# Kernel optimization log

Measured on AMD Instinct MI355X. Metric: run time of the kernel, lower is better.

The kernel has to match this reference:

```python
import math
import jax, jax.numpy as jnp
import numpy as np

B, Q, HID = 4, 4, 4096
NH, NKV, HD = 32, 8, 128
GROUPS = NH // NKV
CACHE_LEN = 4096
CACHE_MAX = CACHE_LEN + 512  # prefill_len + max_len(512)
ROPE_THETA = 500000.0
SCALE = 1.0 / math.sqrt(128.0)  # hardcoded softmax_scale in module


def rotate_half(x):
    x1, x2 = jnp.split(x, 2, axis=-1)
    return jnp.concatenate([-x2, x1], axis=-1)


def setup_inputs() -> dict:
    key = jax.random.key(0)
    ks = jax.random.split(key, 8)
    std = 0.02
    # RoPE angles for positions [CACHE_LEN, CACHE_LEN+Q)
    pos = (CACHE_LEN + jnp.arange(Q)).astype(jnp.float32)
    inv_freq = 1.0 / (ROPE_THETA ** (jnp.arange(0, HD, 2, dtype=jnp.float32) / HD))
    freqs = pos[:, None] * inv_freq[None, :]            # [Q, HD/2]
    emb = jnp.concatenate([freqs, freqs], axis=-1)      # [Q, HD]
    cos = jnp.broadcast_to(jnp.cos(emb)[None], (B, Q, HD)).astype(jnp.float32)
    sin = jnp.broadcast_to(jnp.sin(emb)[None], (B, Q, HD)).astype(jnp.float32)
    return {
        "hidden_states": jax.random.normal(ks[0], (B, Q, HID), jnp.float32),
        "cos": cos,
        "sin": sin,
        "K_Cache": jax.random.normal(ks[1], (B, NKV, CACHE_MAX, HD), jnp.float32) * 0.5,
        "V_Cache": jax.random.normal(ks[2], (B, NKV, CACHE_MAX, HD), jnp.float32) * 0.5,
        "Wq": jax.random.normal(ks[3], (NH * HD, HID), jnp.float32) * std,
        "Wk": jax.random.normal(ks[4], (NKV * HD, HID), jnp.float32) * std,
        "Wv": jax.random.normal(ks[5], (NKV * HD, HID), jnp.float32) * std,
        "Wo": jax.random.normal(ks[6], (HID, NH * HD), jnp.float32) * std,
        "cache_lens": int(CACHE_LEN),
    }


def reference(hidden_states, cos, sin, K_Cache, V_Cache, Wq, Wk, Wv, Wo, cache_lens):
    b, q, _ = hidden_states.shape
    # projections (torch Linear: x @ W.T), reshape to [b, h, q, d]
    qs = jnp.einsum('bsh,oh->bso', hidden_states, Wq).reshape(b, q, NH, HD).transpose(0, 2, 1, 3)
    ks = jnp.einsum('bsh,oh->bso', hidden_states, Wk).reshape(b, q, NKV, HD).transpose(0, 2, 1, 3)
    vs = jnp.einsum('bsh,oh->bso', hidden_states, Wv).reshape(b, q, NKV, HD).transpose(0, 2, 1, 3)
    # RoPE, unsqueeze_dim=1 (head axis)
    c, s = cos[:, None, :, :], sin[:, None, :, :]
    qs = qs * c + rotate_half(qs) * s
    ks = ks * c + rotate_half(ks) * s
    # scatter new K/V into the cache at offset cache_lens
    K_Cache = K_Cache.at[:, :, cache_lens:cache_lens + q, :].set(ks)
    V_Cache = V_Cache.at[:, :, cache_lens:cache_lens + q, :].set(vs)
    # K_total/V_total = cache prefix ++ fresh keys/values; GQA repeat
    K_total = jnp.repeat(jnp.concatenate([K_Cache[:, :, :cache_lens, :], ks], axis=2), GROUPS, axis=1)
    V_total = jnp.repeat(jnp.concatenate([V_Cache[:, :, :cache_lens, :], vs], axis=2), GROUPS, axis=1)
    scores = jnp.einsum('bhqd,bhkd->bhqk', qs, K_total) * SCALE
    # causal mask over the appended q tokens, cache prefix fully visible
    tri = jnp.triu(jnp.ones((q, q), bool), 1)
    mask = jnp.concatenate([jnp.zeros((q, cache_lens), bool), tri], axis=1)
    scores = jnp.where(mask[None, None], -jnp.inf, scores)
    attn = jax.nn.softmax(scores.astype(jnp.float32), axis=-1).astype(V_total.dtype)
    out = jnp.einsum('bhqk,bhkd->bhqd', attn, V_total)
    out = out.transpose(0, 2, 1, 3).reshape(b, q, NH * HD)
    return jnp.einsum('bsh,oh->bso', out, Wo)
```

## Files before the change

kernel.cpp:

```cpp
#include <hip/hip_runtime.h>
#include <hip/hip_fp16.h>
#include <math.h>

#define HIDK 4096
#define NHQ 32
#define HD 128
#define CMAX 4608
#define CLEN 4096
#define NCH 32
#define SCALE 0.08838834764831845f

__device__ __forceinline__ float4 ld4(const float* p) { return *reinterpret_cast<const float4*>(p); }
__device__ __forceinline__ float dot4(float4 a, float4 b) { return a.x*b.x + a.y*b.y + a.z*b.z + a.w*b.w; }

__global__ __launch_bounds__(256) void gemm3_kernel(
    const float* __restrict__ X,
    const float* __restrict__ W1, const float* __restrict__ W2, const float* __restrict__ W3,
    int n1, int n2,
    float* __restrict__ o1, int os1,
    float* __restrict__ o2, int os2,
    float* __restrict__ o3, int os3)
{
  __shared__ float Xs[2][16][256];

  const int tid = threadIdx.x, lane = tid & 63, w = tid >> 6;
  const int o = blockIdx.x * 8 + w * 2;

  const float* Wb; float* ob; int os;
  if (o < n1)           { Wb = W1 + (size_t)o * HIDK;            ob = o1 + o;            os = os1; }
  else if (o < n1 + n2) { const int f = o - n1;      Wb = W2 + (size_t)f * HIDK; ob = o2 + f; os = os2; }
  else                  { const int f = o - n1 - n2; Wb = W3 + (size_t)f * HIDK; ob = o3 + f; os = os3; }

  const int strow = tid >> 6;
  const int stcol = (tid & 63) * 4;

  float acc0[16], acc1[16];
  #pragma unroll
  for (int b = 0; b < 16; ++b) { acc0[b] = 0.f; acc1[b] = 0.f; }

  #pragma unroll
  for (int j = 0; j < 4; ++j)
    *(float4*)&Xs[0][strow + j * 4][stcol] = ld4(X + (size_t)(strow + j * 4) * HIDK + stcol);

  int cur = 0;
  #pragma unroll 2
  for (int kt = 0; kt < 16; ++kt) {
    const float4 w0 = ld4(Wb + (size_t)kt * 256 + lane * 4);
    const float4 w1 = ld4(Wb + HIDK + (size_t)kt * 256 + lane * 4);
    float4 g[4];
    if (kt < 15) {
      #pragma unroll
      for (int j = 0; j < 4; ++j)
        g[j] = ld4(X + (size_t)(strow + j * 4) * HIDK + (kt + 1) * 256 + stcol);
    }
    __syncthreads();
    #pragma unroll
    for (int b = 0; b < 16; ++b) {
      const float4 x4 = *(const float4*)&Xs[cur][b][lane * 4];
      acc0[b] += dot4(x4, w0);
      acc1[b] += dot4(x4, w1);
    }
    if (kt < 15) {
      #pragma unroll
      for (int j = 0; j < 4; ++j)
        *(float4*)&Xs[cur ^ 1][strow + j * 4][stcol] = g[j];
    }
    cur ^= 1;
  }

  #pragma unroll
  for (int m = 1; m < 64; m <<= 1)
    #pragma unroll
    for (int b = 0; b < 16; ++b) {
      acc0[b] += __shfl_xor(acc0[b], m, 64);
      acc1[b] += __shfl_xor(acc1[b], m, 64);
    }
  if (lane == 0) {
    #pragma unroll
    for (int b = 0; b < 16; ++b) {
      ob[(size_t)b * os]     = acc0[b];
      ob[(size_t)b * os + 1] = acc1[b];
    }
  }
}

__global__ __launch_bounds__(256) void qt_prep_kernel(
    const float* __restrict__ qraw, const float* __restrict__ cosp,
    const float* __restrict__ sinp, float* __restrict__ qt)
{
  const int e = blockIdx.x * 256 + threadIdx.x;
  const int r = e & 15;
  const int d = (e >> 4) & 127;
  const int bkv = e >> 11;
  const int b = bkv >> 3, kv = bkv & 7;
  const int s = r & 3, hl = r >> 2;
  const float* qp = qraw + (size_t)(b * 4 + s) * HIDK + (kv * 4 + hl) * HD;
  const float c  = cosp[(b * 4 + s) * HD + d];
  const float sn = sinp[(b * 4 + s) * HD + d];
  const float sgn = (d < 64) ? -1.f : 1.f;
  qt[e] = (qp[d] * c + sgn * qp[d ^ 64] * sn) * SCALE;
}

__global__ __launch_bounds__(128) void attn3_kernel(
    const float* __restrict__ qt, const float* __restrict__ Kc, const float* __restrict__ Vc,
    __half* __restrict__ partOh, float* __restrict__ partM, float* __restrict__ partL)
{
  __shared__ float Plds[2][16][66];
  __shared__ float Oex[16][132];
  __shared__ float MLe[32];

  const int tid = threadIdx.x, lane = tid & 63, w = tid >> 6;
  const int chunk = blockIdx.x & 31, bkv = blockIdx.x >> 5;
  const int b = bkv >> 3, kv = bkv & 7;
  const int p0 = chunk * 128 + w * 64;

  const float* qtb = qt + (size_t)bkv * 2048;
  const float* Kp  = Kc + ((size_t)bkv * CMAX + p0 + lane) * HD;

  float sc[16];
  #pragma unroll
  for (int r = 0; r < 16; ++r) sc[r] = 0.f;
  #pragma unroll 4
  for (int d4 = 0; d4 < 32; ++d4) {
    const float4 k4 = ld4(Kp + d4 * 4);
    #pragma unroll
    for (int r = 0; r < 16; ++r) sc[r] += k4.x * qtb[(d4 * 4 + 0) * 16 + r];
    #pragma unroll
    for (int r = 0; r < 16; ++r) sc[r] += k4.y * qtb[(d4 * 4 + 1) * 16 + r];
    #pragma unroll
    for (int r = 0; r < 16; ++r) sc[r] += k4.z * qtb[(d4 * 4 + 2) * 16 + r];
    #pragma unroll
    for (int r = 0; r < 16; ++r) sc[r] += k4.w * qtb[(d4 * 4 + 3) * 16 + r];
  }

  float m[16], l[16];
  #pragma unroll
  for (int r = 0; r < 16; ++r) {
    float mx = sc[r];
    #pragma unroll
    for (int st = 1; st < 64; st <<= 1) mx = fmaxf(mx, __shfl_xor(mx, st, 64));
    const float p = __expf(sc[r] - mx);
    float ls = p;
    #pragma unroll
    for (int st = 1; st < 64; st <<= 1) ls += __shfl_xor(ls, st, 64);
    m[r] = mx; l[r] = ls;
    Plds[w][r][lane] = p;
  }

  const int dsub = lane & 31, par = lane >> 5;
  const float* Vp = Vc + ((size_t)bkv * CMAX + p0 + par) * HD + dsub * 4;
  float4 o[16];
  #pragma unroll
  for (int r = 0; r < 16; ++r) o[r] = make_float4(0.f, 0.f, 0.f, 0.f);
  #pragma unroll 4
  for (int i = 0; i < 32; ++i) {
    const float4 v4 = ld4(Vp + (size_t)(2 * i) * HD);
    #pragma unroll
    for (int r = 0; r < 16; ++r) {
      const float p = Plds[w][r][2 * i + par];
      o[r].x += p * v4.x; o[r].y += p * v4.y; o[r].z += p * v4.z; o[r].w += p * v4.w;
    }
  }
  #pragma unroll
  for (int r = 0; r < 16; ++r) {
    o[r].x += __shfl_xor(o[r].x, 32, 64);
    o[r].y += __shfl_xor(o[r].y, 32, 64);
    o[r].z += __shfl_xor(o[r].z, 32, 64);
    o[r].w += __shfl_xor(o[r].w, 32, 64);
  }

  if (w == 1) {
    if (lane < 32) {
      #pragma unroll
      for (int r = 0; r < 16; ++r) *(float4*)&Oex[r][dsub * 4] = o[r];
    }
    if (lane == 0) {
      #pragma unroll
      for (int r = 0; r < 16; ++r) { MLe[r] = m[r]; MLe[16 + r] = l[r]; }
    }
  }
  __syncthreads();
  if (w == 0 && lane < 32) {
    #pragma unroll
    for (int r = 0; r < 16; ++r) {
      const float m1 = MLe[r], l1 = MLe[16 + r];
      const float M  = fmaxf(m[r], m1);
      const float a0 = __expf(m[r] - M), a1 = __expf(m1 - M);
      const float4 o1 = *(const float4*)&Oex[r][dsub * 4];
      const float ox = a0 * o[r].x + a1 * o1.x;
      const float oy = a0 * o[r].y + a1 * o1.y;
      const float oz = a0 * o[r].z + a1 * o1.z;
      const float ow = a0 * o[r].w + a1 * o1.w;
      const int row = (b * NHQ + kv * 4 + (r >> 2)) * 4 + (r & 3);
      const size_t idx = ((size_t)row * NCH + chunk) * HD + dsub * 4;
      *(__half2*)&partOh[idx]     = __floats2half2_rn(ox, oy);
      *(__half2*)&partOh[idx + 2] = __floats2half2_rn(oz, ow);
      if (dsub == 0) {
        partM[row * NCH + chunk] = M;
        partL[row * NCH + chunk] = a0 * l[r] + a1 * l1;
      }
    }
  }
}

__global__ __launch_bounds__(64) void combine_kernel(
    const float* __restrict__ qt, const float* __restrict__ kraw, const float* __restrict__ vraw,
    const float* __restrict__ cosp, const float* __restrict__ sinp,
    const __half* __restrict__ partOh, const float* __restrict__ partM, const float* __restrict__ partL,
    float* __restrict__ attn)
{
  const int bid = blockIdx.x;
  const int s = bid & 3;
  const int h = (bid >> 2) & 31;
  const int b = bid >> 7;
  const int kv = h >> 2;
  const int lane = threadIdx.x;
  const int d0 = lane * 2;

  float M = -INFINITY;
  #pragma unroll 4
  for (int c = 0; c < NCH; ++c) M = fmaxf(M, partM[bid * NCH + c]);

  const int rloc = (h & 3) * 4 + s;
  const float qr0 = qt[((size_t)(b * 8 + kv) * 128 + d0) * 16 + rloc];
  const float qr1 = qt[((size_t)(b * 8 + kv) * 128 + d0 + 1) * 16 + rloc];

  float sj[4] = {0.f, 0.f, 0.f, 0.f};
  float Mp = M;
  #pragma unroll
  for (int j = 0; j < 4; ++j) {
    if (j <= s) {
      const float* kp = kraw + (size_t)(b * 4 + j) * 1024 + kv * HD;
      const float c0 = cosp[(b * 4 + j) * HD + d0],     sn0 = sinp[(b * 4 + j) * HD + d0];
      const float c1 = cosp[(b * 4 + j) * HD + d0 + 1], sn1 = sinp[(b * 4 + j) * HD + d0 + 1];
      const float sg0 = (d0 < 64) ? -1.f : 1.f;
      const float sg1 = ((d0 + 1) < 64) ? -1.f : 1.f;
      const float kr0 = kp[d0] * c0 + sg0 * kp[d0 ^ 64] * sn0;
      const float kr1 = kp[d0 + 1] * c1 + sg1 * kp[(d0 + 1) ^ 64] * sn1;
      float part = qr0 * kr0 + qr1 * kr1;
      #pragma unroll
      for (int m = 1; m < 64; m <<= 1) part += __shfl_xor(part, m, 64);
      sj[j] = part;
      Mp = fmaxf(Mp, part);
    }
  }

  float ltot = 0.f, O0 = 0.f, O1 = 0.f;
  #pragma unroll 4
  for (int c = 0; c < NCH; ++c) {
    const float a = __expf(partM[bid * NCH + c] - Mp);
    ltot += partL[bid * NCH + c] * a;
    const float2 v = __half22float2(*(const __half2*)&partOh[((size_t)bid * NCH + c) * HD + d0]);
    O0 += a * v.x;
    O1 += a * v.y;
  }
  #pragma unroll
  for (int j = 0; j < 4; ++j) {
    if (j <= s) {
      const float e = __expf(sj[j] - Mp);
      ltot += e;
      const float* vp = vraw + (size_t)(b * 4 + j) * 1024 + kv * HD + d0;
      O0 += e * vp[0];
      O1 += e * vp[1];
    }
  }
  const float inv = 1.f / ltot;
  *(float2*)&attn[(size_t)(b * 4 + s) * HIDK + h * HD + d0] = make_float2(O0 * inv, O1 * inv);
}

extern "C" void kernel_launch(void* const* d_in, const int* in_sizes, int n_in,
                              void* d_out, int out_size, void* d_ws, size_t ws_size,
                              hipStream_t stream)
{
  const float* hid  = (const float*)d_in[0];
  const float* cosp = (const float*)d_in[1];
  const float* sinp = (const float*)d_in[2];
  const float* Kc   = (const float*)d_in[3];
  const float* Vc   = (const float*)d_in[4];
  const float* Wq   = (const float*)d_in[5];
  const float* Wk   = (const float*)d_in[6];
  const float* Wv   = (const float*)d_in[7];
  const float* Wo   = (const float*)d_in[8];
  float* out = (float*)d_out;

  float* ws    = (float*)d_ws;
  float*  kraw   = ws;
  float*  vraw   = ws + 16384;
  float*  attn   = ws + 32768;
  float*  qt     = ws + 98304;
  float*  qraw   = ws + 163840;
  float*  partM  = ws + 229376;
  float*  partL  = ws + 245760;
  __half* partOh = (__half*)(ws + 262144);

  gemm3_kernel<<<768, 256, 0, stream>>>(hid, Wq, Wk, Wv, 4096, 1024,
                                        qraw, 4096, kraw, 1024, vraw, 1024);
  qt_prep_kernel<<<256, 256, 0, stream>>>(qraw, cosp, sinp, qt);
  attn3_kernel<<<1024, 128, 0, stream>>>(qt, Kc, Vc, partOh, partM, partL);
  combine_kernel<<<512, 64, 0, stream>>>(qt, kraw, vraw, cosp, sinp,
                                         partOh, partM, partL, attn);
  gemm3_kernel<<<512, 256, 0, stream>>>(attn, Wo, Wo, Wo, 4096, 0,
                                        out, 4096, out, 4096, out, 4096);
}
```

Measured before the change: 121.4 us.

## Stage Q in LDS, transpose qt layout, and software-prefetch K/V in attention

Switches the rotated-Q buffer to a row-major [row][d] layout and stages each block's Q tile in shared memory, so QK dot products read float4 vectors from LDS instead of scalar global loads. K and V loads are double-buffered in registers so the next slice is in flight while the current one is used. The P buffer is transposed so the PV loop reads four probabilities per LDS access. The cost is higher register pressure from the prefetch buffers, which may reduce occupancy.

```diff
diff --git a/kernel.cpp b/kernel.cpp
--- a/kernel.cpp
+++ b/kernel.cpp
@@ -89,8 +89,8 @@
     const float* __restrict__ sinp, float* __restrict__ qt)
 {
   const int e = blockIdx.x * 256 + threadIdx.x;
-  const int r = e & 15;
-  const int d = (e >> 4) & 127;
+  const int d = e & 127;
+  const int r = (e >> 7) & 15;
   const int bkv = e >> 11;
   const int b = bkv >> 3, kv = bkv & 7;
   const int s = r & 3, hl = r >> 2;
@@ -101,11 +101,12 @@
   qt[e] = (qp[d] * c + sgn * qp[d ^ 64] * sn) * SCALE;
 }
 
-__global__ __launch_bounds__(128) void attn3_kernel(
+__global__ __launch_bounds__(128) void attn4_kernel(
     const float* __restrict__ qt, const float* __restrict__ Kc, const float* __restrict__ Vc,
     __half* __restrict__ partOh, float* __restrict__ partM, float* __restrict__ partL)
 {
-  __shared__ float Plds[2][16][66];
+  __shared__ float qsh[16][128];
+  __shared__ float P[2][64][20];
   __shared__ float Oex[16][132];
   __shared__ float MLe[32];
 
@@ -114,24 +115,48 @@
   const int b = bkv >> 3, kv = bkv & 7;
   const int p0 = chunk * 128 + w * 64;
 
-  const float* qtb = qt + (size_t)bkv * 2048;
-  const float* Kp  = Kc + ((size_t)bkv * CMAX + p0 + lane) * HD;
-
+  #pragma unroll
+  for (int j = 0; j < 4; ++j) {
+    const int fi = (tid + j * 128) * 4;
+    *(float4*)&qsh[0][fi] = ld4(qt + (size_t)bkv * 2048 + fi);
+  }
+  __syncthreads();
+
+  const float* Kp = Kc + ((size_t)bkv * CMAX + p0 + lane) * HD;
   float sc[16];
   #pragma unroll
   for (int r = 0; r < 16; ++r) sc[r] = 0.f;
-  #pragma unroll 4
-  for (int d4 = 0; d4 < 32; ++d4) {
-    const float4 k4 = ld4(Kp + d4 * 4);
-    #pragma unroll
-    for (int r = 0; r < 16; ++r) sc[r] += k4.x * qtb[(d4 * 4 + 0) * 16 + r];
-    #pragma unroll
-    for (int r = 0; r < 16; ++r) sc[r] += k4.y * qtb[(d4 * 4 + 1) * 16 + r];
-    #pragma unroll
-    for (int r = 0; r < 16; ++r) sc[r] += k4.z * qtb[(d4 * 4 + 2) * 16 + r];
-    #pragma unroll
-    for (int r = 0; r < 16; ++r) sc[r] += k4.w * qtb[(d4 * 4 + 3) * 16 + r];
-  }
+
+  float4 kbuf[8];
+  #pragma unroll
+  for (int i = 0; i < 8; ++i) kbuf[i] = ld4(Kp + i * 4);
+
+  #pragma unroll
+  for (int sb = 0; sb < 4; ++sb) {
+    float4 kn[8];
+    if (sb < 3) {
+      #pragma unroll
+      for (int i = 0; i < 8; ++i) kn[i] = ld4(Kp + ((sb + 1) * 8 + i) * 4);
+    }
+    #pragma unroll
+    for (int i = 0; i < 8; ++i) {
+      const int d4 = sb * 8 + i;
+      const float4 k4 = kbuf[i];
+      #pragma unroll
+      for (int r = 0; r < 16; ++r)
+        sc[r] += dot4(k4, *(const float4*)&qsh[r][d4 * 4]);
+    }
+    if (sb < 3) {
+      #pragma unroll
+      for (int i = 0; i < 8; ++i) kbuf[i] = kn[i];
+    }
+  }
+
+  const int dsub = lane & 31, par = lane >> 5;
+  const float* Vp = Vc + ((size_t)bkv * CMAX + p0 + par) * HD + dsub * 4;
+  float4 vbuf[4];
+  #pragma unroll
+  for (int i = 0; i < 4; ++i) vbuf[i] = ld4(Vp + (size_t)(2 * i) * HD);
 
   float m[16], l[16];
   #pragma unroll
@@ -144,21 +169,36 @@
     #pragma unroll
     for (int st = 1; st < 64; st <<= 1) ls += __shfl_xor(ls, st, 64);
     m[r] = mx; l[r] = ls;
-    Plds[w][r][lane] = p;
-  }
-
-  const int dsub = lane & 31, par = lane >> 5;
-  const float* Vp = Vc + ((size_t)bkv * CMAX + p0 + par) * HD + dsub * 4;
+    P[w][lane][r] = p;
+  }
+
   float4 o[16];
   #pragma unroll
   for (int r = 0; r < 16; ++r) o[r] = make_float4(0.f, 0.f, 0.f, 0.f);
-  #pragma unroll 4
-  for (int i = 0; i < 32; ++i) {
-    const float4 v4 = ld4(Vp + (size_t)(2 * i) * HD);
-    #pragma unroll
-    for (int r = 0; r < 16; ++r) {
-      const float p = Plds[w][r][2 * i + par];
-      o[r].x += p * v4.x; o[r].y += p * v4.y; o[r].z += p * v4.z; o[r].w += p * v4.w;
+
+  #pragma unroll
+  for (int sb = 0; sb < 8; ++sb) {
+    float4 vn[4];
+    if (sb < 7) {
+      #pragma unroll
+      for (int i = 0; i < 4; ++i) vn[i] = ld4(Vp + (size_t)(2 * ((sb + 1) * 4 + i)) * HD);
+    }
+    #pragma unroll
+    for (int i = 0; i < 4; ++i) {
+      const int pc = 2 * (sb * 4 + i) + par;
+      const float4 v4 = vbuf[i];
+      #pragma unroll
+      for (int rq = 0; rq < 4; ++rq) {
+        const float4 p4 = *(const float4*)&P[w][pc][rq * 4];
+        o[rq*4+0].x += p4.x * v4.x; o[rq*4+0].y += p4.x * v4.y; o[rq*4+0].z += p4.x * v4.z; o[rq*4+0].w += p4.x * v4.w;
+        o[rq*4+1].x += p4.y * v4.x; o[rq*4+1].y += p4.y * v4.y; o[rq*4+1].z += p4.y * v4.z; o[rq*4+1].w += p4.y * v4.w;
+        o[rq*4+2].x += p4.z * v4.x; o[rq*4+2].y += p4.z * v4.y; o[rq*4+2].z += p4.z * v4.z; o[rq*4+2].w += p4.z * v4.w;
+        o[rq*4+3].x += p4.w * v4.x; o[rq*4+3].y += p4.w * v4.y; o[rq*4+3].z += p4.w * v4.z; o[rq*4+3].w += p4.w * v4.w;
+      }
+    }
+    if (sb < 7) {
+      #pragma unroll
+      for (int i = 0; i < 4; ++i) vbuf[i] = vn[i];
     }
   }
   #pragma unroll
@@ -222,8 +262,8 @@
   for (int c = 0; c < NCH; ++c) M = fmaxf(M, partM[bid * NCH + c]);
 
   const int rloc = (h & 3) * 4 + s;
-  const float qr0 = qt[((size_t)(b * 8 + kv) * 128 + d0) * 16 + rloc];
-  const float qr1 = qt[((size_t)(b * 8 + kv) * 128 + d0 + 1) * 16 + rloc];
+  const float qr0 = qt[((size_t)(b * 8 + kv) * 16 + rloc) * 128 + d0];
+  const float qr1 = qt[((size_t)(b * 8 + kv) * 16 + rloc) * 128 + d0 + 1];
 
   float sj[4] = {0.f, 0.f, 0.f, 0.f};
   float Mp = M;
@@ -296,7 +336,7 @@
   gemm3_kernel<<<768, 256, 0, stream>>>(hid, Wq, Wk, Wv, 4096, 1024,
                                         qraw, 4096, kraw, 1024, vraw, 1024);
   qt_prep_kernel<<<256, 256, 0, stream>>>(qraw, cosp, sinp, qt);
-  attn3_kernel<<<1024, 128, 0, stream>>>(qt, Kc, Vc, partOh, partM, partL);
+  attn4_kernel<<<1024, 128, 0, stream>>>(qt, Kc, Vc, partOh, partM, partL);
   combine_kernel<<<512, 64, 0, stream>>>(qt, kraw, vraw, cosp, sinp,
                                          partOh, partM, partL, attn);
   gemm3_kernel<<<512, 256, 0, stream>>>(attn, Wo, Wo, Wo, 4096, 0,
```

New measurement: 111.3 us. 8.3% less time.

## Stage K/V tiles in swizzled LDS and split query rows across waves

Applied to the files above, without the earlier changes.

The attention kernel now loads each 64-position K and V tile cooperatively into shared memory with an XOR swizzle, and keeps the query tile in LDS in a row-major layout. Each wave handles 8 of the 16 query rows over the full 128-position chunk using an online softmax, instead of each wave taking half the positions for all 16 rows and merging at the end. The q layout is transposed in the prep and combine kernels to match. This trades direct coalesced global loads and register-held K for more LDS traffic and several block barriers, but it removes the cross-wave merge and lowers register pressure.

```diff
diff --git a/kernel.cpp b/kernel.cpp
--- a/kernel.cpp
+++ b/kernel.cpp
@@ -12,6 +12,7 @@
 
 __device__ __forceinline__ float4 ld4(const float* p) { return *reinterpret_cast<const float4*>(p); }
 __device__ __forceinline__ float dot4(float4 a, float4 b) { return a.x*b.x + a.y*b.y + a.z*b.z + a.w*b.w; }
+__device__ __forceinline__ int kvidx(int pos, int dq) { return pos * 128 + (dq ^ ((pos & 7) << 2)); }
 
 __global__ __launch_bounds__(256) void gemm3_kernel(
     const float* __restrict__ X,
@@ -89,8 +90,8 @@
     const float* __restrict__ sinp, float* __restrict__ qt)
 {
   const int e = blockIdx.x * 256 + threadIdx.x;
-  const int r = e & 15;
-  const int d = (e >> 4) & 127;
+  const int d = e & 127;
+  const int r = (e >> 7) & 15;
   const int bkv = e >> 11;
   const int b = bkv >> 3, kv = bkv & 7;
   const int s = r & 3, hl = r >> 2;
@@ -101,103 +102,124 @@
   qt[e] = (qp[d] * c + sgn * qp[d ^ 64] * sn) * SCALE;
 }
 
-__global__ __launch_bounds__(128) void attn3_kernel(
+__global__ __launch_bounds__(128) void attn5_kernel(
     const float* __restrict__ qt, const float* __restrict__ Kc, const float* __restrict__ Vc,
     __half* __restrict__ partOh, float* __restrict__ partM, float* __restrict__ partL)
 {
-  __shared__ float Plds[2][16][66];
-  __shared__ float Oex[16][132];
-  __shared__ float MLe[32];
+  __shared__ float qsh[16][128];
+  __shared__ float KV[64 * 128];
+  __shared__ float P[64][20];
 
   const int tid = threadIdx.x, lane = tid & 63, w = tid >> 6;
   const int chunk = blockIdx.x & 31, bkv = blockIdx.x >> 5;
   const int b = bkv >> 3, kv = bkv & 7;
-  const int p0 = chunk * 128 + w * 64;
-
-  const float* qtb = qt + (size_t)bkv * 2048;
-  const float* Kp  = Kc + ((size_t)bkv * CMAX + p0 + lane) * HD;
-
-  float sc[16];
-  #pragma unroll
-  for (int r = 0; r < 16; ++r) sc[r] = 0.f;
-  #pragma unroll 4
-  for (int d4 = 0; d4 < 32; ++d4) {
-    const float4 k4 = ld4(Kp + d4 * 4);
-    #pragma unroll
-    for (int r = 0; r < 16; ++r) sc[r] += k4.x * qtb[(d4 * 4 + 0) * 16 + r];
-    #pragma unroll
-    for (int r = 0; r < 16; ++r) sc[r] += k4.y * qtb[(d4 * 4 + 1) * 16 + r];
-    #pragma unroll
-    for (int r = 0; r < 16; ++r) sc[r] += k4.z * qtb[(d4 * 4 + 2) * 16 + r];
-    #pragma unroll
-    for (int r = 0; r < 16; ++r) sc[r] += k4.w * qtb[(d4 * 4 + 3) * 16 + r];
-  }
-
-  float m[16], l[16];
-  #pragma unroll
-  for (int r = 0; r < 16; ++r) {
-    float mx = sc[r];
-    #pragma unroll
-    for (int st = 1; st < 64; st <<= 1) mx = fmaxf(mx, __shfl_xor(mx, st, 64));
-    const float p = __expf(sc[r] - mx);
-    float ls = p;
-    #pragma unroll
-    for (int st = 1; st < 64; st <<= 1) ls += __shfl_xor(ls, st, 64);
-    m[r] = mx; l[r] = ls;
-    Plds[w][r][lane] = p;
-  }
-
-  const int dsub = lane & 31, par = lane >> 5;
-  const float* Vp = Vc + ((size_t)bkv * CMAX + p0 + par) * HD + dsub * 4;
-  float4 o[16];
-  #pragma unroll
-  for (int r = 0; r < 16; ++r) o[r] = make_float4(0.f, 0.f, 0.f, 0.f);
-  #pragma unroll 4
-  for (int i = 0; i < 32; ++i) {
-    const float4 v4 = ld4(Vp + (size_t)(2 * i) * HD);
-    #pragma unroll
-    for (int r = 0; r < 16; ++r) {
-      const float p = Plds[w][r][2 * i + par];
-      o[r].x += p * v4.x; o[r].y += p * v4.y; o[r].z += p * v4.z; o[r].w += p * v4.w;
-    }
-  }
-  #pragma unroll
-  for (int r = 0; r < 16; ++r) {
+  const int p0 = chunk * 128;
+
+  const float* Kb = Kc + ((size_t)bkv * CMAX + p0) * HD;
+  const float* Vb = Vc + ((size_t)bkv * CMAX + p0) * HD;
+
+  const int dsub = tid & 31;
+  const int rp   = tid >> 5;
+
+  #pragma unroll
+  for (int j = 0; j < 4; ++j) {
+    const int fi = (tid + j * 128) * 4;
+    *(float4*)&qsh[0][fi] = ld4(qt + (size_t)bkv * 2048 + fi);
+  }
+  #pragma unroll
+  for (int i = 0; i < 16; ++i) {
+    const int pos = i * 4 + rp;
+    *(float4*)&KV[kvidx(pos, dsub * 4)] = ld4(Kb + (size_t)pos * HD + dsub * 4);
+  }
+  __syncthreads();
+
+  float m[8], l[8];
+  float4 o[8];
+  #pragma unroll
+  for (int r = 0; r < 8; ++r) { m[r] = -INFINITY; l[r] = 0.f; o[r] = make_float4(0.f, 0.f, 0.f, 0.f); }
+
+  const int par = lane >> 5, dc = lane & 31;
+
+  #pragma unroll
+  for (int t = 0; t < 2; ++t) {
+    float sc[8];
+    #pragma unroll
+    for (int r = 0; r < 8; ++r) sc[r] = 0.f;
+    #pragma unroll 8
+    for (int d4 = 0; d4 < 32; ++d4) {
+      const float4 k4 = *(const float4*)&KV[kvidx(lane, d4 * 4)];
+      #pragma unroll
+      for (int r = 0; r < 8; ++r)
+        sc[r] += dot4(k4, *(const float4*)&qsh[w * 8 + r][d4 * 4]);
+    }
+    #pragma unroll
+    for (int r = 0; r < 8; ++r) {
+      float mx = sc[r];
+      #pragma unroll
+      for (int st = 1; st < 64; st <<= 1) mx = fmaxf(mx, __shfl_xor(mx, st, 64));
+      const float mn = fmaxf(m[r], mx);
+      const float p  = __expf(sc[r] - mn);
+      float ls = p;
+      #pragma unroll
+      for (int st = 1; st < 64; st <<= 1) ls += __shfl_xor(ls, st, 64);
+      const float scal = __expf(m[r] - mn);
+      m[r] = mn;
+      l[r] = l[r] * scal + ls;
+      o[r].x *= scal; o[r].y *= scal; o[r].z *= scal; o[r].w *= scal;
+      P[lane][w * 8 + r] = p;
+    }
+    __syncthreads();
+    #pragma unroll
+    for (int i = 0; i < 16; ++i) {
+      const int pos = i * 4 + rp;
+      *(float4*)&KV[kvidx(pos, dsub * 4)] = ld4(Vb + (size_t)(t * 64 + pos) * HD + dsub * 4);
+    }
+    __syncthreads();
+    #pragma unroll 8
+    for (int i = 0; i < 32; ++i) {
+      const int pos = 2 * i + par;
+      const float4 v4 = *(const float4*)&KV[kvidx(pos, dc * 4)];
+      const float4 pa = *(const float4*)&P[pos][w * 8];
+      const float4 pb = *(const float4*)&P[pos][w * 8 + 4];
+      o[0].x += pa.x * v4.x; o[0].y += pa.x * v4.y; o[0].z += pa.x * v4.z; o[0].w += pa.x * v4.w;
+      o[1].x += pa.y * v4.x; o[1].y += pa.y * v4.y; o[1].z += pa.y * v4.z; o[1].w += pa.y * v4.w;
+      o[2].x += pa.z * v4.x; o[2].y += pa.z * v4.y; o[2].z += pa.z * v4.z; o[2].w += pa.z * v4.w;
+      o[3].x += pa.w * v4.x; o[3].y += pa.w * v4.y; o[3].z += pa.w * v4.z; o[3].w += pa.w * v4.w;
+      o[4].x += pb.x * v4.x; o[4].y += pb.x * v4.y; o[4].z += pb.x * v4.z; o[4].w += pb.x * v4.w;
+      o[5].x += pb.y * v4.x; o[5].y += pb.y * v4.y; o[5].z += pb.y * v4.z; o[5].w += pb.y * v4.w;
+      o[6].x += pb.z * v4.x; o[6].y += pb.z * v4.y; o[6].z += pb.z * v4.z; o[6].w += pb.z * v4.w;
+      o[7].x += pb.w * v4.x; o[7].y += pb.w * v4.y; o[7].z += pb.w * v4.z; o[7].w += pb.w * v4.w;
+    }
+    if (t == 0) {
+      __syncthreads();
+      #pragma unroll
+      for (int i = 0; i < 16; ++i) {
+        const int pos = i * 4 + rp;
+        *(float4*)&KV[kvidx(pos, dsub * 4)] = ld4(Kb + (size_t)(64 + pos) * HD + dsub * 4);
+      }
+      __syncthreads();
+    }
+  }
+
+  #pragma unroll
+  for (int r = 0; r < 8; ++r) {
     o[r].x += __shfl_xor(o[r].x, 32, 64);
     o[r].y += __shfl_xor(o[r].y, 32, 64);
     o[r].z += __shfl_xor(o[r].z, 32, 64);
     o[r].w += __shfl_xor(o[r].w, 32, 64);
   }
-
-  if (w == 1) {
-    if (lane < 32) {
-      #pragma unroll
-      for (int r = 0; r < 16; ++r) *(float4*)&Oex[r][dsub * 4] = o[r];
-    }
-    if (lane == 0) {
-      #pragma unroll
-      for (int r = 0; r < 16; ++r) { MLe[r] = m[r]; MLe[16 + r] = l[r]; }
-    }
-  }
-  __syncthreads();
-  if (w == 0 && lane < 32) {
-    #pragma unroll
-    for (int r = 0; r < 16; ++r) {
-      const float m1 = MLe[r], l1 = MLe[16 + r];
-      const float M  = fmaxf(m[r], m1);
-      const float a0 = __expf(m[r] - M), a1 = __expf(m1 - M);
-      const float4 o1 = *(const float4*)&Oex[r][dsub * 4];
-      const float ox = a0 * o[r].x + a1 * o1.x;
-      const float oy = a0 * o[r].y + a1 * o1.y;
-      const float oz = a0 * o[r].z + a1 * o1.z;
-      const float ow = a0 * o[r].w + a1 * o1.w;
-      const int row = (b * NHQ + kv * 4 + (r >> 2)) * 4 + (r & 3);
-      const size_t idx = ((size_t)row * NCH + chunk) * HD + dsub * 4;
-      *(__half2*)&partOh[idx]     = __floats2half2_rn(ox, oy);
-      *(__half2*)&partOh[idx + 2] = __floats2half2_rn(oz, ow);
-      if (dsub == 0) {
-        partM[row * NCH + chunk] = M;
-        partL[row * NCH + chunk] = a0 * l[r] + a1 * l1;
+  if (lane < 32) {
+    #pragma unroll
+    for (int r = 0; r < 8; ++r) {
+      const int rg = w * 8 + r;
+      const int hl = rg >> 2, s = rg & 3;
+      const int row = (b * NHQ + kv * 4 + hl) * 4 + s;
+      const size_t idx = ((size_t)row * NCH + chunk) * HD + dc * 4;
+      *(__half2*)&partOh[idx]     = __floats2half2_rn(o[r].x, o[r].y);
+      *(__half2*)&partOh[idx + 2] = __floats2half2_rn(o[r].z, o[r].w);
+      if (dc == 0) {
+        partM[row * NCH + chunk] = m[r];
+        partL[row * NCH + chunk] = l[r];
       }
     }
   }
@@ -222,8 +244,8 @@
   for (int c = 0; c < NCH; ++c) M = fmaxf(M, partM[bid * NCH + c]);
 
   const int rloc = (h & 3) * 4 + s;
-  const float qr0 = qt[((size_t)(b * 8 + kv) * 128 + d0) * 16 + rloc];
-  const float qr1 = qt[((size_t)(b * 8 + kv) * 128 + d0 + 1) * 16 + rloc];
+  const float qr0 = qt[((size_t)(b * 8 + kv) * 16 + rloc) * 128 + d0];
+  const float qr1 = qt[((size_t)(b * 8 + kv) * 16 + rloc) * 128 + d0 + 1];
 
   float sj[4] = {0.f, 0.f, 0.f, 0.f};
   float Mp = M;
@@ -296,7 +318,7 @@
   gemm3_kernel<<<768, 256, 0, stream>>>(hid, Wq, Wk, Wv, 4096, 1024,
                                         qraw, 4096, kraw, 1024, vraw, 1024);
   qt_prep_kernel<<<256, 256, 0, stream>>>(qraw, cosp, sinp, qt);
-  attn3_kernel<<<1024, 128, 0, stream>>>(qt, Kc, Vc, partOh, partM, partL);
+  attn5_kernel<<<1024, 128, 0, stream>>>(qt, Kc, Vc, partOh, partM, partL);
   combine_kernel<<<512, 64, 0, stream>>>(qt, kraw, vraw, cosp, sinp,
                                          partOh, partM, partL, attn);
   gemm3_kernel<<<512, 256, 0, stream>>>(attn, Wo, Wo, Wo, 4096, 0,
```

After: 134.1 us. 10.5% more time.

## Restructure split-K attention with 4 waves splitting head dim and positions

Applied to the files above, without the earlier changes.

The attention kernel moves to 256 threads per block. QK^T is split across two waves per position half, each covering half the head dimension, with partial scores reduced through shared memory. Softmax max and sum are combined across waves in shared memory, and the PV product splits the head dimension across four waves with software-prefetched V loads. The q layout changes to row-major per query row so float4 loads work, and combine_kernel indexing is updated to match. The aim is more parallelism and memory-level overlap per chunk, at the cost of extra syncs and shuffle reductions.

```diff
diff --git a/kernel.cpp b/kernel.cpp
--- a/kernel.cpp
+++ b/kernel.cpp
@@ -89,8 +89,8 @@
     const float* __restrict__ sinp, float* __restrict__ qt)
 {
   const int e = blockIdx.x * 256 + threadIdx.x;
-  const int r = e & 15;
-  const int d = (e >> 4) & 127;
+  const int d = e & 127;
+  const int r = (e >> 7) & 15;
   const int bkv = e >> 11;
   const int b = bkv >> 3, kv = bkv & 7;
   const int s = r & 3, hl = r >> 2;
@@ -101,104 +101,137 @@
   qt[e] = (qp[d] * c + sgn * qp[d ^ 64] * sn) * SCALE;
 }
 
-__global__ __launch_bounds__(128) void attn3_kernel(
+__global__ __launch_bounds__(256, 4) void attn7_kernel(
     const float* __restrict__ qt, const float* __restrict__ Kc, const float* __restrict__ Vc,
     __half* __restrict__ partOh, float* __restrict__ partM, float* __restrict__ partL)
 {
-  __shared__ float Plds[2][16][66];
-  __shared__ float Oex[16][132];
-  __shared__ float MLe[32];
+  __shared__ float Pex[2][128][21];
+  __shared__ float P[128][21];
+  __shared__ float Mex[2][16];
+  __shared__ float Lex[2][16];
 
   const int tid = threadIdx.x, lane = tid & 63, w = tid >> 6;
+  const int ph = w >> 1, sub = w & 1;
   const int chunk = blockIdx.x & 31, bkv = blockIdx.x >> 5;
   const int b = bkv >> 3, kv = bkv & 7;
-  const int p0 = chunk * 128 + w * 64;
-
-  const float* qtb = qt + (size_t)bkv * 2048;
-  const float* Kp  = Kc + ((size_t)bkv * CMAX + p0 + lane) * HD;
-
-  float sc[16];
-  #pragma unroll
-  for (int r = 0; r < 16; ++r) sc[r] = 0.f;
-  #pragma unroll 4
-  for (int d4 = 0; d4 < 32; ++d4) {
-    const float4 k4 = ld4(Kp + d4 * 4);
-    #pragma unroll
-    for (int r = 0; r < 16; ++r) sc[r] += k4.x * qtb[(d4 * 4 + 0) * 16 + r];
-    #pragma unroll
-    for (int r = 0; r < 16; ++r) sc[r] += k4.y * qtb[(d4 * 4 + 1) * 16 + r];
-    #pragma unroll
-    for (int r = 0; r < 16; ++r) sc[r] += k4.z * qtb[(d4 * 4 + 2) * 16 + r];
-    #pragma unroll
-    for (int r = 0; r < 16; ++r) sc[r] += k4.w * qtb[(d4 * 4 + 3) * 16 + r];
-  }
-
-  float m[16], l[16];
+  const int p0 = chunk * 128;
+
+  const float* Kb = Kc + ((size_t)bkv * CMAX + p0) * HD;
+  const float* Vb = Vc + ((size_t)bkv * CMAX + p0) * HD;
+  const float* qb = qt + (size_t)bkv * 2048;
+
+  const int pos = ph * 64 + lane;
+
+  {
+    const float* Kp = Kb + (size_t)pos * HD + sub * 64;
+    float ps[16];
+    #pragma unroll
+    for (int r = 0; r < 16; ++r) ps[r] = 0.f;
+
+    float4 kb4[4];
+    #pragma unroll
+    for (int j = 0; j < 4; ++j) kb4[j] = ld4(Kp + j * 4);
+
+    #pragma unroll
+    for (int i = 0; i < 16; ++i) {
+      const float4 k4 = kb4[i & 3];
+      if (i < 12) kb4[i & 3] = ld4(Kp + (i + 4) * 4);
+      #pragma unroll
+      for (int r = 0; r < 16; ++r) {
+        const float4 q4 = ld4(qb + r * 128 + sub * 64 + i * 4);
+        ps[r] += dot4(k4, q4);
+      }
+    }
+    #pragma unroll
+    for (int r = 0; r < 16; ++r) Pex[sub][pos][r] = ps[r];
+  }
+  __syncthreads();
+
+  float sc[8], mreg[8];
+  #pragma unroll
+  for (int r = 0; r < 8; ++r) {
+    const int row = sub * 8 + r;
+    sc[r] = Pex[0][pos][row] + Pex[1][pos][row];
+    float mx = sc[r];
+    #pragma unroll
+    for (int st = 1; st < 64; st <<= 1) mx = fmaxf(mx, __shfl_xor(mx, st, 64));
+    mreg[r] = mx;
+  }
+  if (lane == 0) {
+    #pragma unroll
+    for (int r = 0; r < 8; ++r) Mex[ph][sub * 8 + r] = mreg[r];
+  }
+  __syncthreads();
+
+  {
+    float lreg[8];
+    #pragma unroll
+    for (int r = 0; r < 8; ++r) {
+      const int row = sub * 8 + r;
+      const float mc = fmaxf(Mex[0][row], Mex[1][row]);
+      const float p = __expf(sc[r] - mc);
+      float ls = p;
+      #pragma unroll
+      for (int st = 1; st < 64; st <<= 1) ls += __shfl_xor(ls, st, 64);
+      lreg[r] = ls;
+      P[pos][row] = p;
+    }
+    if (lane == 0) {
+      #pragma unroll
+      for (int r = 0; r < 8; ++r) Lex[ph][sub * 8 + r] = lreg[r];
+    }
+  }
+  __syncthreads();
+
+  if (ph == 0 && lane < 8) {
+    const int row = sub * 8 + lane;
+    const int hl = row >> 2, s = row & 3;
+    const int grow = (b * NHQ + kv * 4 + hl) * 4 + s;
+    partM[grow * NCH + chunk] = fmaxf(Mex[0][row], Mex[1][row]);
+    partL[grow * NCH + chunk] = Lex[0][row] + Lex[1][row];
+  }
+
+  const int dc = lane & 7, pp = lane >> 3;
+  const float* Vp = Vb + (size_t)pp * HD + w * 32 + dc * 4;
+
+  float4 o[16];
+  #pragma unroll
+  for (int r = 0; r < 16; ++r) o[r] = make_float4(0.f, 0.f, 0.f, 0.f);
+
+  float4 vb4[4];
+  #pragma unroll
+  for (int j = 0; j < 4; ++j) vb4[j] = ld4(Vp + (size_t)(8 * j) * HD);
+
+  #pragma unroll
+  for (int i = 0; i < 16; ++i) {
+    const float4 v4 = vb4[i & 3];
+    if (i < 12) vb4[i & 3] = ld4(Vp + (size_t)(8 * (i + 4)) * HD);
+    const int pv = 8 * i + pp;
+    #pragma unroll
+    for (int r = 0; r < 16; ++r) {
+      const float p = P[pv][r];
+      o[r].x += p * v4.x; o[r].y += p * v4.y; o[r].z += p * v4.z; o[r].w += p * v4.w;
+    }
+  }
+
   #pragma unroll
   for (int r = 0; r < 16; ++r) {
-    float mx = sc[r];
-    #pragma unroll
-    for (int st = 1; st < 64; st <<= 1) mx = fmaxf(mx, __shfl_xor(mx, st, 64));
-    const float p = __expf(sc[r] - mx);
-    float ls = p;
-    #pragma unroll
-    for (int st = 1; st < 64; st <<= 1) ls += __shfl_xor(ls, st, 64);
-    m[r] = mx; l[r] = ls;
-    Plds[w][r][lane] = p;
-  }
-
-  const int dsub = lane & 31, par = lane >> 5;
-  const float* Vp = Vc + ((size_t)bkv * CMAX + p0 + par) * HD + dsub * 4;
-  float4 o[16];
-  #pragma unroll
-  for (int r = 0; r < 16; ++r) o[r] = make_float4(0.f, 0.f, 0.f, 0.f);
-  #pragma unroll 4
-  for (int i = 0; i < 32; ++i) {
-    const float4 v4 = ld4(Vp + (size_t)(2 * i) * HD);
+    #pragma unroll
+    for (int st = 8; st < 64; st <<= 1) {
+      o[r].x += __shfl_xor(o[r].x, st, 64);
+      o[r].y += __shfl_xor(o[r].y, st, 64);
+      o[r].z += __shfl_xor(o[r].z, st, 64);
+      o[r].w += __shfl_xor(o[r].w, st, 64);
+    }
+  }
+  if (pp == 0) {
     #pragma unroll
     for (int r = 0; r < 16; ++r) {
-      const float p = Plds[w][r][2 * i + par];
-      o[r].x += p * v4.x; o[r].y += p * v4.y; o[r].z += p * v4.z; o[r].w += p * v4.w;
-    }
-  }
-  #pragma unroll
-  for (int r = 0; r < 16; ++r) {
-    o[r].x += __shfl_xor(o[r].x, 32, 64);
-    o[r].y += __shfl_xor(o[r].y, 32, 64);
-    o[r].z += __shfl_xor(o[r].z, 32, 64);
-    o[r].w += __shfl_xor(o[r].w, 32, 64);
-  }
-
-  if (w == 1) {
-    if (lane < 32) {
-      #pragma unroll
-      for (int r = 0; r < 16; ++r) *(float4*)&Oex[r][dsub * 4] = o[r];
-    }
-    if (lane == 0) {
-      #pragma unroll
-      for (int r = 0; r < 16; ++r) { MLe[r] = m[r]; MLe[16 + r] = l[r]; }
-    }
-  }
-  __syncthreads();
-  if (w == 0 && lane < 32) {
-    #pragma unroll
-    for (int r = 0; r < 16; ++r) {
-      const float m1 = MLe[r], l1 = MLe[16 + r];
-      const float M  = fmaxf(m[r], m1);
-      const float a0 = __expf(m[r] - M), a1 = __expf(m1 - M);
-      const float4 o1 = *(const float4*)&Oex[r][dsub * 4];
-      const float ox = a0 * o[r].x + a1 * o1.x;
-      const float oy = a0 * o[r].y + a1 * o1.y;
-      const float oz = a0 * o[r].z + a1 * o1.z;
-      const float ow = a0 * o[r].w + a1 * o1.w;
-      const int row = (b * NHQ + kv * 4 + (r >> 2)) * 4 + (r & 3);
-      const size_t idx = ((size_t)row * NCH + chunk) * HD + dsub * 4;
-      *(__half2*)&partOh[idx]     = __floats2half2_rn(ox, oy);
-      *(__half2*)&partOh[idx + 2] = __floats2half2_rn(oz, ow);
-      if (dsub == 0) {
-        partM[row * NCH + chunk] = M;
-        partL[row * NCH + chunk] = a0 * l[r] + a1 * l1;
-      }
+      const int hl = r >> 2, s = r & 3;
+      const int grow = (b * NHQ + kv * 4 + hl) * 4 + s;
+      const size_t idx = ((size_t)grow * NCH + chunk) * HD + w * 32 + dc * 4;
+      *(__half2*)&partOh[idx]     = __floats2half2_rn(o[r].x, o[r].y);
+      *(__half2*)&partOh[idx + 2] = __floats2half2_rn(o[r].z, o[r].w);
     }
   }
 }
@@ -222,8 +255,8 @@
   for (int c = 0; c < NCH; ++c) M = fmaxf(M, partM[bid * NCH + c]);
 
   const int rloc = (h & 3) * 4 + s;
-  const float qr0 = qt[((size_t)(b * 8 + kv) * 128 + d0) * 16 + rloc];
-  const float qr1 = qt[((size_t)(b * 8 + kv) * 128 + d0 + 1) * 16 + rloc];
+  const float qr0 = qt[((size_t)(b * 8 + kv) * 16 + rloc) * 128 + d0];
+  const float qr1 = qt[((size_t)(b * 8 + kv) * 16 + rloc) * 128 + d0 + 1];
 
   float sj[4] = {0.f, 0.f, 0.f, 0.f};
   float Mp = M;
@@ -296,7 +329,7 @@
   gemm3_kernel<<<768, 256, 0, stream>>>(hid, Wq, Wk, Wv, 4096, 1024,
                                         qraw, 4096, kraw, 1024, vraw, 1024);
   qt_prep_kernel<<<256, 256, 0, stream>>>(qraw, cosp, sinp, qt);
-  attn3_kernel<<<1024, 128, 0, stream>>>(qt, Kc, Vc, partOh, partM, partL);
+  attn7_kernel<<<1024, 256, 0, stream>>>(qt, Kc, Vc, partOh, partM, partL);
   combine_kernel<<<512, 64, 0, stream>>>(qt, kraw, vraw, cosp, sinp,
                                          partOh, partM, partL, attn);
   gemm3_kernel<<<512, 256, 0, stream>>>(attn, Wo, Wo, Wo, 4096, 0,
```

Result: slower. 276.1 us (+127.5%).
